# Kernel optimization log

Measured on AMD Instinct MI355X. Metric: run time of the kernel, lower is better.

## Reference

```python
import jax, jax.numpy as jnp
import numpy as np

N_LAYERS = 8
DILATIONS = [1, 2, 1, 2, 1, 2, 1, 2]
K_HOPS = 3
BN = 13248   # batch(64) * n_nodes(207), merged as in the torch module
L = 13       # 12 history steps + 1; shrinks by sum(dilations)=12 across layers
E = 211968   # BN * avg_degree(16)


def _conv1d(x, w, b, dil):
    # x: (BN, Cin, L), w: (Cout, Cin, 2) kernel-2 dilated conv, VALID (causal shrink)
    y = jax.lax.conv_general_dilated(x, w, (1,), 'VALID', rhs_dilation=(dil,),
                                     dimension_numbers=('NCH', 'OIH', 'NCH'))
    return y + b[None, :, None]


def setup_inputs() -> dict:
    key = jax.random.key(0)
    ks = jax.random.split(key, 20)
    s = 0.1  # keep activations in a sane range
    return {
        'x': jax.random.normal(ks[0], (BN, L, 2), jnp.float32),
        'edge_src': jax.random.randint(ks[1], (E,), 0, BN),
        'edge_dst': jax.random.randint(ks[2], (E,), 0, BN),
        'edge_w': jax.random.uniform(ks[3], (E,), jnp.float32),
        'init_w': s * jax.random.normal(ks[4], (2, 32), jnp.float32),
        'init_b': s * jax.random.normal(ks[5], (32,), jnp.float32),
        'filt_w': s * jax.random.normal(ks[6], (8, 32, 32, 2), jnp.float32),
        'filt_b': s * jax.random.normal(ks[7], (8, 32), jnp.float32),
        'gate_w': s * jax.random.normal(ks[8], (8, 32, 32, 2), jnp.float32),
        'gate_b': s * jax.random.normal(ks[9], (8, 32), jnp.float32),
        'gcn_w': s * jax.random.normal(ks[10], (8, 6, 32, 32), jnp.float32),
        'gcn_b': s * jax.random.normal(ks[11], (8, 32), jnp.float32),
        'skip_w': s * jax.random.normal(ks[12], (8, 256, 32), jnp.float32),
        'skip_b': s * jax.random.normal(ks[13], (8, 256), jnp.float32),
        'out0_w': s * jax.random.normal(ks[14], (256, 512), jnp.float32),
        'out0_b': s * jax.random.normal(ks[15], (512,), jnp.float32),
        'out1_w': s * jax.random.normal(ks[16], (512, 12), jnp.float32),
        'out1_b': s * jax.random.normal(ks[17], (12,), jnp.float32),
    }


def reference(x, edge_src, edge_dst, edge_w, init_w, init_b,
              filt_w, filt_b, gate_w, gate_b, gcn_w, gcn_b,
              skip_w, skip_b, out0_w, out0_b, out1_w, out1_b):
    # init linear: (BN, L, 2) -> (BN, L, 32) -> (BN, 32, L)
    h = (x @ init_w + init_b).transpose(0, 2, 1)
    # per-hop edge weights: elementwise powers of the transition weights
    # (faithful to repo's dense_to_sparse(transition ** k)); bck = transposed edges
    adjs = [(edge_src, edge_dst, edge_w ** k) for k in range(1, K_HOPS + 1)] + \
           [(edge_dst, edge_src, edge_w ** k) for k in range(1, K_HOPS + 1)]
    skip = None
    for l in range(N_LAYERS):
        d = DILATIONS[l]
        res = h
        # Gated TCN: tanh(filter) * sigmoid(gate), seq shrinks by d
        t = jnp.tanh(_conv1d(h, filt_w[l], filt_b[l], d)) * \
            jax.nn.sigmoid(_conv1d(h, gate_w[l], gate_b[l], d))
        # Diffusion conv: sum over 6 adjacency types of A_w (x W_a)
        xt = t.transpose(0, 2, 1)  # (BN, L', 32)
        g = jnp.zeros_like(xt)
        for a, (src, dst, w) in enumerate(adjs):
            msg = (xt @ gcn_w[l, a])[src] * w[:, None, None]  # (E, L', 32)
            g = g + jax.ops.segment_sum(msg, dst, num_segments=BN)
        h = g.transpose(0, 2, 1) + gcn_b[l][None, :, None]  # (BN, 32, L')
        # residual connection (align shrunk sequence)
        h = h + res[:, :, -h.shape[-1]:]
        # skip conv (1x1) on last timestep, accumulated
        sc = h[:, :, -1] @ skip_w[l].T + skip_b[l]  # (BN, 256)
        skip = sc if skip is None else skip + sc
    out = jax.nn.relu(skip)
    out = jax.nn.relu(out @ out0_w + out0_b)
    return out @ out1_w + out1_b  # (BN, 12)
```

## Files before the change

kernel.cpp:

```cpp
#include <hip/hip_runtime.h>

#define BN 13248
#define NE 211968

typedef __attribute__((ext_vector_type(8))) short bf16x8;
typedef __attribute__((ext_vector_type(4))) float f32x4;

__device__ __forceinline__ f32x4 mfma16(bf16x8 a, bf16x8 b, f32x4 c) {
  return __builtin_amdgcn_mfma_f32_16x16x32_bf16(a, b, c, 0, 0, 0);
}

__device__ __forceinline__ unsigned short to_bf16(float v) {
  unsigned bits = __float_as_uint(v);
  return (unsigned short)((bits + 0x7FFFu + ((bits >> 16) & 1u)) >> 16);
}

__device__ __forceinline__ float fast_tanh(float x) {
  float e2 = __expf(2.f * x);
  return 1.f - 2.f / (e2 + 1.f);
}
__device__ __forceinline__ float fast_sig(float x) {
  return 1.f / (1.f + __expf(-x));
}

__global__ void k_count(const int* __restrict__ src, const int* __restrict__ dst,
                        int* __restrict__ cur_f, int* __restrict__ cur_b) {
  int e = blockIdx.x * 256 + threadIdx.x;
  if (e < NE) {
    atomicAdd(&cur_f[dst[e]], 1);
    atomicAdd(&cur_b[src[e]], 1);
  }
}

__global__ void k_scan(int* __restrict__ cur_f, int* __restrict__ row_f,
                       int* __restrict__ cur_b, int* __restrict__ row_b) {
  __shared__ int sdata[1024];
  int tid = threadIdx.x;
  for (int which = 0; which < 2; ++which) {
    int* cnt = which ? cur_b : cur_f;
    int* row = which ? row_b : row_f;
    int base = tid * 13;
    int vals[13];
    int tot = 0;
    for (int k = 0; k < 13; ++k) {
      int idx = base + k;
      int v = (idx < BN) ? cnt[idx] : 0;
      vals[k] = v; tot += v;
    }
    sdata[tid] = tot;
    __syncthreads();
    for (int off = 1; off < 1024; off <<= 1) {
      int add = (tid >= off) ? sdata[tid - off] : 0;
      __syncthreads();
      sdata[tid] += add;
      __syncthreads();
    }
    int running = sdata[tid] - tot;
    for (int k = 0; k < 13; ++k) {
      int idx = base + k;
      if (idx < BN) { row[idx] = running; cnt[idx] = running; running += vals[k]; }
    }
    if (tid == 1023) row[BN] = sdata[1023];
    __syncthreads();
  }
}

__global__ void k_fill(const int* __restrict__ src, const int* __restrict__ dst,
                       const float* __restrict__ w,
                       int* __restrict__ cur_f, int2* __restrict__ ce_f,
                       int* __restrict__ cur_b, int2* __restrict__ ce_b) {
  int e = blockIdx.x * 256 + threadIdx.x;
  if (e < NE) {
    int s = src[e], t = dst[e];
    int wb = __float_as_int(w[e]);
    int p = atomicAdd(&cur_f[t], 1); ce_f[p] = make_int2(s, wb);
    int q = atomicAdd(&cur_b[s], 1); ce_b[q] = make_int2(t, wb);
  }
}

__global__ void k_init(const float* __restrict__ x, const float* __restrict__ iw,
                       const float* __restrict__ ib, float* __restrict__ h) {
  int idx = blockIdx.x * 256 + threadIdx.x;
  if (idx >= BN * 13 * 32) return;
  int c = idx & 31;
  int r = idx >> 5;
  int n = r % BN;
  int tau = r / BN;
  float x0 = x[(n * 13 + tau) * 2 + 0];
  float x1 = x[(n * 13 + tau) * 2 + 1];
  h[idx] = fmaf(x0, iw[c], fmaf(x1, iw[32 + c], ib[c]));
}

__global__ void k_pack(const float* __restrict__ skip_w, const float* __restrict__ skip_b,
                       const float* __restrict__ w0, const float* __restrict__ w1,
                       const float* __restrict__ gcn_w,
                       unsigned short* __restrict__ SWb, unsigned short* __restrict__ W0T,
                       unsigned short* __restrict__ W1T, float* __restrict__ bsum,
                       unsigned short* __restrict__ GgT) {
  int id = blockIdx.x * 256 + threadIdx.x;
  if (id < 65536) {
    int j = id >> 8, k = id & 255;
    SWb[id] = to_bf16(skip_w[((k >> 5) * 256 + j) * 32 + (k & 31)]);
  }
  if (id < 131072) {
    int jo = id >> 8, k = id & 255;
    W0T[id] = to_bf16(w0[k * 512 + jo]);
  }
  if (id < 8192) {
    int n = id >> 9, k = id & 511;
    W1T[id] = (n < 12) ? to_bf16(w1[k * 12 + n]) : (unsigned short)0;
  }
  if (id < 256) {
    float s = 0.f;
    for (int l = 0; l < 8; ++l) s += skip_b[l * 256 + id];
    bsum[id] = s;
  }
  if (id < 49152) {
    int l = id / 6144, rem = id % 6144;
    int co = rem / 192, k = rem % 192;
    int a = k >> 5, ci = k & 31;
    GgT[id] = to_bf16(gcn_w[((l * 6 + a) * 32 + ci) * 32 + co]);
  }
}

template<int LIN, int D, int TPAD>
__global__ __launch_bounds__(256) void k_tcn(const float* __restrict__ h_in, unsigned short* __restrict__ t_out,
    const float* __restrict__ fw, const float* __restrict__ fb,
    const float* __restrict__ gw, const float* __restrict__ gb) {
  constexpr int LOUT = LIN - D;
  __shared__ __align__(16) float wq[32 * 32 * 4];
  __shared__ float hl[8][LIN * 32];
  int tid = threadIdx.x;
  for (int f = tid; f < 4096; f += 256) {
    int e = f & 3, co = (f >> 2) & 31, ci = f >> 7;
    const float* srcw = (e < 2) ? fw : gw;
    wq[f] = srcw[(co * 32 + ci) * 2 + (e & 1)];
  }
  int n0 = blockIdx.x * 8;
  for (int i = tid; i < 8 * LIN * 32; i += 256) {
    int c = i & 31, r = i >> 5;
    int nl = r / LIN, tau = r % LIN;
    hl[nl][tau * 32 + c] = h_in[(tau * BN + n0 + nl) * 32 + c];
  }
  __syncthreads();
  int nl = tid >> 5, co = tid & 31;
  int n = n0 + nl;
  float accf[LOUT], accg[LOUT];
  float fbv = fb[co], gbv = gb[co];
#pragma unroll
  for (int j = 0; j < LOUT; ++j) { accf[j] = fbv; accg[j] = gbv; }
#pragma unroll
  for (int ci = 0; ci < 32; ++ci) {
    float4 wv = *(const float4*)&wq[(ci * 32 + co) * 4];
    float xr[LIN];
#pragma unroll
    for (int t = 0; t < LIN; ++t) xr[t] = hl[nl][t * 32 + ci];
#pragma unroll
    for (int j = 0; j < LOUT; ++j) {
      accf[j] = fmaf(xr[j], wv.x, accf[j]);
      accf[j] = fmaf(xr[j + D], wv.y, accf[j]);
      accg[j] = fmaf(xr[j], wv.z, accg[j]);
      accg[j] = fmaf(xr[j + D], wv.w, accg[j]);
    }
  }
#pragma unroll
  for (int j = 0; j < TPAD; ++j) {
    float v = (j < LOUT) ? fast_tanh(accf[j < LOUT ? j : 0]) * fast_sig(accg[j < LOUT ? j : 0]) : 0.f;
    t_out[(n * TPAD + j) * 32 + co] = (j < LOUT) ? to_bf16(v) : (unsigned short)0;
  }
}

__device__ __forceinline__ void bf4_fma3(uint2 u, float w1, float w2, float w3,
                                         float4* A0, float4* A1, float4* A2) {
  float v0 = __uint_as_float(u.x << 16);
  float v1 = __uint_as_float(u.x & 0xFFFF0000u);
  float v2 = __uint_as_float(u.y << 16);
  float v3 = __uint_as_float(u.y & 0xFFFF0000u);
  A0->x = fmaf(w1, v0, A0->x); A0->y = fmaf(w1, v1, A0->y);
  A0->z = fmaf(w1, v2, A0->z); A0->w = fmaf(w1, v3, A0->w);
  A1->x = fmaf(w2, v0, A1->x); A1->y = fmaf(w2, v1, A1->y);
  A1->z = fmaf(w2, v2, A1->z); A1->w = fmaf(w2, v3, A1->w);
  A2->x = fmaf(w3, v0, A2->x); A2->y = fmaf(w3, v1, A2->y);
  A2->z = fmaf(w3, v2, A2->z); A2->w = fmaf(w3, v3, A2->w);
}

template<int TPAD, int NT>
__device__ __forceinline__ void gather_dir(const unsigned short* __restrict__ t_in,
    int e0, int e1, const int2* __restrict__ ce, int rowoff0, float4 (*A)[NT]) {
  constexpr int EB = (NT >= 3) ? 2 : 4;
  int e = e0;
  for (; e + EB <= e1; e += EB) {
    int2 c[EB];
    uint2 u[EB][NT];
#pragma unroll
    for (int k = 0; k < EB; ++k) c[k] = ce[e + k];
#pragma unroll
    for (int k = 0; k < EB; ++k) {
      const unsigned short* p = t_in + c[k].x * (TPAD * 32) + rowoff0;
#pragma unroll
      for (int j = 0; j < NT; ++j) u[k][j] = *(const uint2*)(p + j * 32);
    }
#pragma unroll
    for (int k = 0; k < EB; ++k) {
      float w1 = __int_as_float(c[k].y);
      float w2 = w1 * w1, w3 = w2 * w1;
#pragma unroll
      for (int j = 0; j < NT; ++j)
        bf4_fma3(u[k][j], w1, w2, w3, &A[0][j], &A[1][j], &A[2][j]);
    }
  }
  for (; e < e1; ++e) {
    int2 c = ce[e];
    float w1 = __int_as_float(c.y);
    float w2 = w1 * w1, w3 = w2 * w1;
    const unsigned short* p = t_in + c.x * (TPAD * 32) + rowoff0;
#pragma unroll
    for (int j = 0; j < NT; ++j) {
      uint2 u = *(const uint2*)(p + j * 32);
      bf4_fma3(u, w1, w2, w3, &A[0][j], &A[1][j], &A[2][j]);
    }
  }
}

#define ZSTRIDE 200

template<int LOUT, int D, int TPAD>
__global__ __launch_bounds__(128, 4) void k_agg(const unsigned short* __restrict__ t_in,
    const float* __restrict__ h_in, float* __restrict__ h_out, float* __restrict__ lastcol,
    const int* __restrict__ row_f, const int2* __restrict__ ce_f,
    const int* __restrict__ row_b, const int2* __restrict__ ce_b,
    const unsigned short* __restrict__ WgT,
    const float* __restrict__ bias) {
  constexpr int NT = TPAD / 4;
  __shared__ __align__(16) unsigned short Zl[4 * TPAD * ZSTRIDE];
  int tid = threadIdx.x;
  int nl = tid >> 5, lane32 = tid & 31;
  int tl = lane32 >> 3;
  int c4 = (lane32 & 7) << 2;
  int n0 = blockIdx.x * 4;
  int n = n0 + nl;
  int rowoff0 = (tl * NT) * 32 + c4;
  int ef0 = row_f[n], ef1 = row_f[n + 1];
  int eb0 = row_b[n], eb1 = row_b[n + 1];
  float4 accf[3][NT], accb[3][NT];
#pragma unroll
  for (int a = 0; a < 3; ++a)
#pragma unroll
    for (int j = 0; j < NT; ++j) {
      accf[a][j] = make_float4(0.f, 0.f, 0.f, 0.f);
      accb[a][j] = make_float4(0.f, 0.f, 0.f, 0.f);
    }
  gather_dir<TPAD, NT>(t_in, ef0, ef1, ce_f, rowoff0, accf);
  gather_dir<TPAD, NT>(t_in, eb0, eb1, ce_b, rowoff0, accb);
#pragma unroll
  for (int j = 0; j < NT; ++j) {
    int m = nl * TPAD + tl * NT + j;
#pragma unroll
    for (int a = 0; a < 3; ++a) {
      ushort4 pf, pb;
      pf.x = to_bf16(accf[a][j].x); pf.y = to_bf16(accf[a][j].y);
      pf.z = to_bf16(accf[a][j].z); pf.w = to_bf16(accf[a][j].w);
      pb.x = to_bf16(accb[a][j].x); pb.y = to_bf16(accb[a][j].y);
      pb.z = to_bf16(accb[a][j].z); pb.w = to_bf16(accb[a][j].w);
      *(ushort4*)(&Zl[m * ZSTRIDE + a * 32 + c4]) = pf;
      *(ushort4*)(&Zl[m * ZSTRIDE + (a + 3) * 32 + c4]) = pb;
    }
  }
  __syncthreads();
  int wave = tid >> 6, lane = tid & 63;
  int m16 = lane & 15, q = lane >> 4;
#pragma unroll
  for (int i = 0; i < NT; ++i) {
    int u = wave * NT + i;
    int mt = u >> 1, nt = u & 1;
    f32x4 dacc = (f32x4){0.f, 0.f, 0.f, 0.f};
#pragma unroll
    for (int ks = 0; ks < 6; ++ks) {
      bf16x8 av = *(const bf16x8*)(&Zl[(mt * 16 + m16) * ZSTRIDE + ks * 32 + q * 8]);
      bf16x8 bv = *(const bf16x8*)(WgT + (nt * 16 + m16) * 192 + ks * 32 + q * 8);
      dacc = mfma16(av, bv, dacc);
    }
    int co = nt * 16 + m16;
    float bco = bias[co];
#pragma unroll
    for (int r = 0; r < 4; ++r) {
      int mm = mt * 16 + q * 4 + r;
      int node = n0 + mm / TPAD;
      int tau = mm % TPAD;
      if (tau < LOUT) {
        float rres = h_in[((tau + D) * BN + node) * 32 + co];
        float o = dacc[r] + bco + rres;
        h_out[(tau * BN + node) * 32 + co] = o;
        if (tau == LOUT - 1) lastcol[node * 32 + co] = o;
      }
    }
  }
}

__device__ __forceinline__ bf16x8 ldsA(const unsigned short* buf, int stride, int row, int ks, int q) {
  int unit = ks * 4 + q;
  int addr = row * stride + ((unit ^ (row & 7)) << 3);
  return *(const bf16x8*)(buf + addr);
}

__global__ __launch_bounds__(256) void k_final(const float* __restrict__ lastcol,
    const unsigned short* __restrict__ SWb, const unsigned short* __restrict__ W0T,
    const unsigned short* __restrict__ W1T, const float* __restrict__ bsum,
    const float* __restrict__ b0, const float* __restrict__ b1,
    float* __restrict__ out) {
  __shared__ __align__(16) unsigned short Z[32 * 256];
  __shared__ __align__(16) unsigned short H[32 * 512];
  int tid = threadIdx.x;
  int wave = tid >> 6, lane = tid & 63;
  int m16 = lane & 15, q = lane >> 4;
  int n0 = blockIdx.x * 32;
#pragma unroll
  for (int it = 0; it < 32; ++it) {
    int id = it * 256 + tid;
    int m = id >> 8, k = id & 255;
    float v = lastcol[((k >> 5) * BN + n0 + m) * 32 + (k & 31)];
    Z[m * 256 + (((k >> 3) ^ (m & 7)) << 3) + (k & 7)] = to_bf16(v);
  }
  __syncthreads();
  f32x4 acc1[2][4];
#pragma unroll
  for (int mt = 0; mt < 2; ++mt)
#pragma unroll
    for (int i = 0; i < 4; ++i) acc1[mt][i] = (f32x4){0.f, 0.f, 0.f, 0.f};
#pragma unroll
  for (int ks = 0; ks < 8; ++ks) {
    bf16x8 a0 = ldsA(Z, 256, m16, ks, q);
    bf16x8 a1 = ldsA(Z, 256, 16 + m16, ks, q);
#pragma unroll
    for (int i = 0; i < 4; ++i) {
      int j = (wave * 4 + i) * 16 + m16;
      bf16x8 b = *(const bf16x8*)(SWb + j * 256 + ks * 32 + q * 8);
      acc1[0][i] = mfma16(a0, b, acc1[0][i]);
      acc1[1][i] = mfma16(a1, b, acc1[1][i]);
    }
  }
  __syncthreads();
#pragma unroll
  for (int i = 0; i < 4; ++i) {
    int j = (wave * 4 + i) * 16 + m16;
    float bs = bsum[j];
#pragma unroll
    for (int mt = 0; mt < 2; ++mt)
#pragma unroll
      for (int r = 0; r < 4; ++r) {
        int row = mt * 16 + q * 4 + r;
        float v = fmaxf(acc1[mt][i][r] + bs, 0.f);
        Z[row * 256 + (((j >> 3) ^ (row & 7)) << 3) + (j & 7)] = to_bf16(v);
      }
  }
  __syncthreads();
  f32x4 acc2[2][8];
#pragma unroll
  for (int mt = 0; mt < 2; ++mt)
#pragma unroll
    for (int i = 0; i < 8; ++i) acc2[mt][i] = (f32x4){0.f, 0.f, 0.f, 0.f};
#pragma unroll
  for (int ks = 0; ks < 8; ++ks) {
    bf16x8 a0 = ldsA(Z, 256, m16, ks, q);
    bf16x8 a1 = ldsA(Z, 256, 16 + m16, ks, q);
#pragma unroll
    for (int i = 0; i < 8; ++i) {
      int jo = (wave * 8 + i) * 16 + m16;
      bf16x8 b = *(const bf16x8*)(W0T + jo * 256 + ks * 32 + q * 8);
      acc2[0][i] = mfma16(a0, b, acc2[0][i]);
      acc2[1][i] = mfma16(a1, b, acc2[1][i]);
    }
  }
#pragma unroll
  for (int i = 0; i < 8; ++i) {
    int jo = (wave * 8 + i) * 16 + m16;
    float b0v = b0[jo];
#pragma unroll
    for (int mt = 0; mt < 2; ++mt)
#pragma unroll
      for (int r = 0; r < 4; ++r) {
        int row = mt * 16 + q * 4 + r;
        float v = fmaxf(acc2[mt][i][r] + b0v, 0.f);
        H[row * 512 + (((jo >> 3) ^ (row & 7)) << 3) + (jo & 7)] = to_bf16(v);
      }
  }
  __syncthreads();
  if (wave < 2) {
    f32x4 acc3 = (f32x4){0.f, 0.f, 0.f, 0.f};
#pragma unroll
    for (int ks = 0; ks < 16; ++ks) {
      bf16x8 a = ldsA(H, 512, wave * 16 + m16, ks, q);
      bf16x8 b = *(const bf16x8*)(W1T + m16 * 512 + ks * 32 + q * 8);
      acc3 = mfma16(a, b, acc3);
    }
    if (m16 < 12) {
      float bv = b1[m16];
#pragma unroll
      for (int r = 0; r < 4; ++r)
        out[(n0 + wave * 16 + q * 4 + r) * 12 + m16] = acc3[r] + bv;
    }
  }
}

extern "C" void kernel_launch(void* const* d_in, const int* in_sizes, int n_in,
                              void* d_out, int out_size, void* d_ws, size_t ws_size,
                              hipStream_t stream) {
  const float* x      = (const float*)d_in[0];
  const int*   esrc   = (const int*)d_in[1];
  const int*   edst   = (const int*)d_in[2];
  const float* ew     = (const float*)d_in[3];
  const float* init_w = (const float*)d_in[4];
  const float* init_b = (const float*)d_in[5];
  const float* filt_w = (const float*)d_in[6];
  const float* filt_b = (const float*)d_in[7];
  const float* gate_w = (const float*)d_in[8];
  const float* gate_b = (const float*)d_in[9];
  const float* gcn_w  = (const float*)d_in[10];
  const float* gcn_b  = (const float*)d_in[11];
  const float* skip_w = (const float*)d_in[12];
  const float* skip_b = (const float*)d_in[13];
  const float* w0     = (const float*)d_in[14];
  const float* b0     = (const float*)d_in[15];
  const float* w1     = (const float*)d_in[16];
  const float* b1     = (const float*)d_in[17];
  float* out = (float*)d_out;

  float* base = (float*)d_ws;
  float* hA      = base;
  float* hB      = hA + 13 * BN * 32;
  float* tbuf    = hB + 13 * BN * 32;
  float* lastcol = tbuf + 12 * BN * 32;
  int* row_f = (int*)(lastcol + 8 * BN * 32);
  int* row_b = row_f + (BN + 1);
  int* cur_f = row_b + (BN + 1);
  int* cur_b = cur_f + BN;
  int2* ce_f = (int2*)(cur_b + BN);
  int2* ce_b = ce_f + NE;
  unsigned short* tbuf_u = (unsigned short*)tbuf;
  unsigned short* SWb = tbuf_u + 16 * BN * 32;
  unsigned short* W0T = SWb + 65536;
  unsigned short* W1T = W0T + 131072;
  float* bsumv = (float*)(W1T + 8192);
  unsigned short* GgT = (unsigned short*)(bsumv + 256);

  hipMemsetAsync(cur_f, 0, 2 * BN * sizeof(int), stream);
  const int egrid = (NE + 255) / 256;
  k_count<<<egrid, 256, 0, stream>>>(esrc, edst, cur_f, cur_b);
  k_scan<<<1, 1024, 0, stream>>>(cur_f, row_f, cur_b, row_b);
  k_fill<<<egrid, 256, 0, stream>>>(esrc, edst, ew, cur_f, ce_f, cur_b, ce_b);
  k_init<<<(BN * 13 * 32 + 255) / 256, 256, 0, stream>>>(x, init_w, init_b, hA);
  k_pack<<<512, 256, 0, stream>>>(skip_w, skip_b, w0, w1, gcn_w, SWb, W0T, W1T, bsumv, GgT);

#define LAYER(l, LIN, DD, TP, hin, hout) \
  k_tcn<LIN, DD, TP><<<BN / 8, 256, 0, stream>>>(hin, tbuf_u, filt_w + l * 2048, filt_b + l * 32, \
                                                 gate_w + l * 2048, gate_b + l * 32); \
  k_agg<LIN - DD, DD, TP><<<BN / 4, 128, 0, stream>>>(tbuf_u, hin, hout, \
      lastcol + l * BN * 32, row_f, ce_f, row_b, ce_b, GgT + l * 6144, gcn_b + l * 32);

  LAYER(0, 13, 1, 12, hA, hB)
  LAYER(1, 12, 2, 12, hB, hA)
  LAYER(2, 10, 1, 12, hA, hB)
  LAYER(3,  9, 2,  8, hB, hA)
  LAYER(4,  7, 1,  8, hA, hB)
  LAYER(5,  6, 2,  4, hB, hA)
  LAYER(6,  4, 1,  4, hA, hB)
  LAYER(7,  3, 2,  4, hB, hA)
#undef LAYER

  k_final<<<BN / 32, 256, 0, stream>>>(lastcol, SWb, W0T, W1T, bsumv, b0, b1, out);
}
```

Before: 759.7 us.

## Fuse next-layer TCN into aggregation kernel and switch gather to packed fp16

Each aggregation kernel now computes the gated TCN of the following layer from the freshly produced h values kept in shared memory. This removes seven separate TCN launches and the global re-read of h. Intermediate t activations and GCN weights move from bf16 to fp16, and the edge gather accumulates with packed half2 FMAs instead of fp32, halving the ALU work per edge. The cost is fp16 accumulation over many edges, which risks precision loss or overflow, more shared memory, and fewer resident blocks because launch bounds drop to 2.

Measured after the change: 740.3 us. -2.6%, faster.

```diff
diff --git a/kernel.cpp b/kernel.cpp
--- a/kernel.cpp
+++ b/kernel.cpp
@@ -1,18 +1,33 @@
 #include <hip/hip_runtime.h>
+#include <hip/hip_fp16.h>
 
 #define BN 13248
 #define NE 211968
+#define ZSTRIDE 200
 
 typedef __attribute__((ext_vector_type(8))) short bf16x8;
+typedef __attribute__((ext_vector_type(8))) _Float16 f16x8;
 typedef __attribute__((ext_vector_type(4))) float f32x4;
 
-__device__ __forceinline__ f32x4 mfma16(bf16x8 a, bf16x8 b, f32x4 c) {
+__device__ __forceinline__ f32x4 mfma16b(bf16x8 a, bf16x8 b, f32x4 c) {
   return __builtin_amdgcn_mfma_f32_16x16x32_bf16(a, b, c, 0, 0, 0);
+}
+__device__ __forceinline__ f32x4 mfma16h(f16x8 a, f16x8 b, f32x4 c) {
+  return __builtin_amdgcn_mfma_f32_16x16x32_f16(a, b, c, 0, 0, 0);
 }
 
 __device__ __forceinline__ unsigned short to_bf16(float v) {
   unsigned bits = __float_as_uint(v);
   return (unsigned short)((bits + 0x7FFFu + ((bits >> 16) & 1u)) >> 16);
+}
+__device__ __forceinline__ unsigned short to_f16(float v) {
+  union { __half h; unsigned short s; } u; u.h = __float2half(v); return u.s;
+}
+__device__ __forceinline__ unsigned h2u(__half2 h) {
+  union { __half2 h; unsigned u; } v; v.h = h; return v.u;
+}
+__device__ __forceinline__ __half2 u2h(unsigned u) {
+  union { unsigned u; __half2 h; } v; v.u = u; return v.h;
 }
 
 __device__ __forceinline__ float fast_tanh(float x) {
@@ -94,9 +109,10 @@
 __global__ void k_pack(const float* __restrict__ skip_w, const float* __restrict__ skip_b,
                        const float* __restrict__ w0, const float* __restrict__ w1,
                        const float* __restrict__ gcn_w,
+                       const float* __restrict__ filt_w, const float* __restrict__ gate_w,
                        unsigned short* __restrict__ SWb, unsigned short* __restrict__ W0T,
                        unsigned short* __restrict__ W1T, float* __restrict__ bsum,
-                       unsigned short* __restrict__ GgT) {
+                       unsigned short* __restrict__ Gg16, uint2* __restrict__ WQ2) {
   int id = blockIdx.x * 256 + threadIdx.x;
   if (id < 65536) {
     int j = id >> 8, k = id & 255;
@@ -119,7 +135,17 @@
     int l = id / 6144, rem = id % 6144;
     int co = rem / 192, k = rem % 192;
     int a = k >> 5, ci = k & 31;
-    GgT[id] = to_bf16(gcn_w[((l * 6 + a) * 32 + ci) * 32 + co]);
+    Gg16[id] = to_f16(gcn_w[((l * 6 + a) * 32 + ci) * 32 + co]);
+  }
+  if (id < 7168) {
+    int l = id / 1024 + 1, rem = id % 1024;
+    int ci = rem >> 5, co = rem & 31;
+    const float* fw = filt_w + l * 2048;
+    const float* gw = gate_w + l * 2048;
+    __half2 a, b;
+    a.x = __float2half(fw[(co * 32 + ci) * 2 + 0]); a.y = __float2half(gw[(co * 32 + ci) * 2 + 0]);
+    b.x = __float2half(fw[(co * 32 + ci) * 2 + 1]); b.y = __float2half(gw[(co * 32 + ci) * 2 + 1]);
+    WQ2[id] = make_uint2(h2u(a), h2u(b));
   }
 }
 
@@ -165,29 +191,16 @@
   }
 #pragma unroll
   for (int j = 0; j < TPAD; ++j) {
-    float v = (j < LOUT) ? fast_tanh(accf[j < LOUT ? j : 0]) * fast_sig(accg[j < LOUT ? j : 0]) : 0.f;
-    t_out[(n * TPAD + j) * 32 + co] = (j < LOUT) ? to_bf16(v) : (unsigned short)0;
-  }
-}
-
-__device__ __forceinline__ void bf4_fma3(uint2 u, float w1, float w2, float w3,
-                                         float4* A0, float4* A1, float4* A2) {
-  float v0 = __uint_as_float(u.x << 16);
-  float v1 = __uint_as_float(u.x & 0xFFFF0000u);
-  float v2 = __uint_as_float(u.y << 16);
-  float v3 = __uint_as_float(u.y & 0xFFFF0000u);
-  A0->x = fmaf(w1, v0, A0->x); A0->y = fmaf(w1, v1, A0->y);
-  A0->z = fmaf(w1, v2, A0->z); A0->w = fmaf(w1, v3, A0->w);
-  A1->x = fmaf(w2, v0, A1->x); A1->y = fmaf(w2, v1, A1->y);
-  A1->z = fmaf(w2, v2, A1->z); A1->w = fmaf(w2, v3, A1->w);
-  A2->x = fmaf(w3, v0, A2->x); A2->y = fmaf(w3, v1, A2->y);
-  A2->z = fmaf(w3, v2, A2->z); A2->w = fmaf(w3, v3, A2->w);
+    unsigned short v = 0;
+    if (j < LOUT) v = to_f16(fast_tanh(accf[j < LOUT ? j : 0]) * fast_sig(accg[j < LOUT ? j : 0]));
+    t_out[(n * TPAD + j) * 32 + co] = v;
+  }
 }
 
 template<int TPAD, int NT>
 __device__ __forceinline__ void gather_dir(const unsigned short* __restrict__ t_in,
-    int e0, int e1, const int2* __restrict__ ce, int rowoff0, float4 (*A)[NT]) {
-  constexpr int EB = (NT >= 3) ? 2 : 4;
+    int e0, int e1, const int2* __restrict__ ce, int rowoff0, __half2* A) {
+  constexpr int EB = 4;
   int e = e0;
   for (; e + EB <= e1; e += EB) {
     int2 c[EB];
@@ -202,38 +215,60 @@
     }
 #pragma unroll
     for (int k = 0; k < EB; ++k) {
-      float w1 = __int_as_float(c[k].y);
-      float w2 = w1 * w1, w3 = w2 * w1;
-#pragma unroll
-      for (int j = 0; j < NT; ++j)
-        bf4_fma3(u[k][j], w1, w2, w3, &A[0][j], &A[1][j], &A[2][j]);
+      float w1 = __int_as_float(c[k].y), w2 = w1 * w1, w3 = w2 * w1;
+      __half2 wh0 = __float2half2_rn(w1), wh1 = __float2half2_rn(w2), wh2 = __float2half2_rn(w3);
+#pragma unroll
+      for (int j = 0; j < NT; ++j) {
+        __half2 v0 = u2h(u[k][j].x), v1 = u2h(u[k][j].y);
+        A[(0 * NT + j) * 2 + 0] = __hfma2(wh0, v0, A[(0 * NT + j) * 2 + 0]);
+        A[(0 * NT + j) * 2 + 1] = __hfma2(wh0, v1, A[(0 * NT + j) * 2 + 1]);
+        A[(1 * NT + j) * 2 + 0] = __hfma2(wh1, v0, A[(1 * NT + j) * 2 + 0]);
+        A[(1 * NT + j) * 2 + 1] = __hfma2(wh1, v1, A[(1 * NT + j) * 2 + 1]);
+        A[(2 * NT + j) * 2 + 0] = __hfma2(wh2, v0, A[(2 * NT + j) * 2 + 0]);
+        A[(2 * NT + j) * 2 + 1] = __hfma2(wh2, v1, A[(2 * NT + j) * 2 + 1]);
+      }
     }
   }
   for (; e < e1; ++e) {
     int2 c = ce[e];
-    float w1 = __int_as_float(c.y);
-    float w2 = w1 * w1, w3 = w2 * w1;
+    float w1 = __int_as_float(c.y), w2 = w1 * w1, w3 = w2 * w1;
+    __half2 wh0 = __float2half2_rn(w1), wh1 = __float2half2_rn(w2), wh2 = __float2half2_rn(w3);
     const unsigned short* p = t_in + c.x * (TPAD * 32) + rowoff0;
 #pragma unroll
     for (int j = 0; j < NT; ++j) {
       uint2 u = *(const uint2*)(p + j * 32);
-      bf4_fma3(u, w1, w2, w3, &A[0][j], &A[1][j], &A[2][j]);
-    }
-  }
-}
-
-#define ZSTRIDE 200
-
-template<int LOUT, int D, int TPAD>
-__global__ __launch_bounds__(128, 4) void k_agg(const unsigned short* __restrict__ t_in,
-    const float* __restrict__ h_in, float* __restrict__ h_out, float* __restrict__ lastcol,
+      __half2 v0 = u2h(u.x), v1 = u2h(u.y);
+      A[(0 * NT + j) * 2 + 0] = __hfma2(wh0, v0, A[(0 * NT + j) * 2 + 0]);
+      A[(0 * NT + j) * 2 + 1] = __hfma2(wh0, v1, A[(0 * NT + j) * 2 + 1]);
+      A[(1 * NT + j) * 2 + 0] = __hfma2(wh1, v0, A[(1 * NT + j) * 2 + 0]);
+      A[(1 * NT + j) * 2 + 1] = __hfma2(wh1, v1, A[(1 * NT + j) * 2 + 1]);
+      A[(2 * NT + j) * 2 + 0] = __hfma2(wh2, v0, A[(2 * NT + j) * 2 + 0]);
+      A[(2 * NT + j) * 2 + 1] = __hfma2(wh2, v1, A[(2 * NT + j) * 2 + 1]);
+    }
+  }
+}
+
+template<int LOUT, int D, int TPAD, int D2, int TPAD2, bool LAST>
+__global__ __launch_bounds__(128, 2) void k_fused(
+    const unsigned short* __restrict__ t_in,
+    const float* __restrict__ h_in, float* __restrict__ h_out,
+    float* __restrict__ lastcol, unsigned short* __restrict__ t_next,
     const int* __restrict__ row_f, const int2* __restrict__ ce_f,
     const int* __restrict__ row_b, const int2* __restrict__ ce_b,
-    const unsigned short* __restrict__ WgT,
-    const float* __restrict__ bias) {
+    const unsigned short* __restrict__ Wg,
+    const float* __restrict__ bias,
+    const uint2* __restrict__ WQn,
+    const float* __restrict__ fbn, const float* __restrict__ gbn) {
   constexpr int NT = TPAD / 4;
+  constexpr int LIN2 = LOUT;
+  constexpr int LOUT2 = LAST ? 1 : (LOUT - D2);
   __shared__ __align__(16) unsigned short Zl[4 * TPAD * ZSTRIDE];
+  __shared__ __align__(16) uint2 wq2s[1024];
+  __shared__ float hbuf[4 * LIN2 * 33];
   int tid = threadIdx.x;
+  if (!LAST) {
+    for (int i = tid; i < 1024; i += 128) wq2s[i] = WQn[i];
+  }
   int nl = tid >> 5, lane32 = tid & 31;
   int tl = lane32 >> 3;
   int c4 = (lane32 & 7) << 2;
@@ -242,28 +277,19 @@
   int rowoff0 = (tl * NT) * 32 + c4;
   int ef0 = row_f[n], ef1 = row_f[n + 1];
   int eb0 = row_b[n], eb1 = row_b[n + 1];
-  float4 accf[3][NT], accb[3][NT];
-#pragma unroll
-  for (int a = 0; a < 3; ++a)
-#pragma unroll
-    for (int j = 0; j < NT; ++j) {
-      accf[a][j] = make_float4(0.f, 0.f, 0.f, 0.f);
-      accb[a][j] = make_float4(0.f, 0.f, 0.f, 0.f);
-    }
-  gather_dir<TPAD, NT>(t_in, ef0, ef1, ce_f, rowoff0, accf);
-  gather_dir<TPAD, NT>(t_in, eb0, eb1, ce_b, rowoff0, accb);
+  __half2 acc[6 * NT * 2];
+  __half2 zero = __float2half2_rn(0.f);
+#pragma unroll
+  for (int i = 0; i < 6 * NT * 2; ++i) acc[i] = zero;
+  gather_dir<TPAD, NT>(t_in, ef0, ef1, ce_f, rowoff0, acc);
+  gather_dir<TPAD, NT>(t_in, eb0, eb1, ce_b, rowoff0, acc + 3 * NT * 2);
 #pragma unroll
   for (int j = 0; j < NT; ++j) {
     int m = nl * TPAD + tl * NT + j;
 #pragma unroll
-    for (int a = 0; a < 3; ++a) {
-      ushort4 pf, pb;
-      pf.x = to_bf16(accf[a][j].x); pf.y = to_bf16(accf[a][j].y);
-      pf.z = to_bf16(accf[a][j].z); pf.w = to_bf16(accf[a][j].w);
-      pb.x = to_bf16(accb[a][j].x); pb.y = to_bf16(accb[a][j].y);
-      pb.z = to_bf16(accb[a][j].z); pb.w = to_bf16(accb[a][j].w);
-      *(ushort4*)(&Zl[m * ZSTRIDE + a * 32 + c4]) = pf;
-      *(ushort4*)(&Zl[m * ZSTRIDE + (a + 3) * 32 + c4]) = pb;
+    for (int a = 0; a < 6; ++a) {
+      uint2 v = make_uint2(h2u(acc[(a * NT + j) * 2 + 0]), h2u(acc[(a * NT + j) * 2 + 1]));
+      *(uint2*)(&Zl[m * ZSTRIDE + a * 32 + c4]) = v;
     }
   }
   __syncthreads();
@@ -276,9 +302,9 @@
     f32x4 dacc = (f32x4){0.f, 0.f, 0.f, 0.f};
 #pragma unroll
     for (int ks = 0; ks < 6; ++ks) {
-      bf16x8 av = *(const bf16x8*)(&Zl[(mt * 16 + m16) * ZSTRIDE + ks * 32 + q * 8]);
-      bf16x8 bv = *(const bf16x8*)(WgT + (nt * 16 + m16) * 192 + ks * 32 + q * 8);
-      dacc = mfma16(av, bv, dacc);
+      f16x8 av = *(const f16x8*)(&Zl[(mt * 16 + m16) * ZSTRIDE + ks * 32 + q * 8]);
+      f16x8 bv = *(const f16x8*)((const _Float16*)Wg + (nt * 16 + m16) * 192 + ks * 32 + q * 8);
+      dacc = mfma16h(av, bv, dacc);
     }
     int co = nt * 16 + m16;
     float bco = bias[co];
@@ -291,8 +317,41 @@
         float rres = h_in[((tau + D) * BN + node) * 32 + co];
         float o = dacc[r] + bco + rres;
         h_out[(tau * BN + node) * 32 + co] = o;
+        hbuf[(mm / TPAD) * (LIN2 * 33) + tau * 33 + co] = o;
         if (tau == LOUT - 1) lastcol[node * 32 + co] = o;
       }
+    }
+  }
+  if (!LAST) {
+    __syncthreads();
+    int co = lane32;
+    float accf[LOUT2], accg[LOUT2];
+    float fbv = fbn[co], gbv = gbn[co];
+#pragma unroll
+    for (int j = 0; j < LOUT2; ++j) { accf[j] = fbv; accg[j] = gbv; }
+    const float* hb = &hbuf[nl * (LIN2 * 33)];
+#pragma unroll
+    for (int ci = 0; ci < 32; ++ci) {
+      uint2 wp = wq2s[ci * 32 + co];
+      __half2 wa = u2h(wp.x), wb = u2h(wp.y);
+      float wf0 = __low2float(wa), wg0 = __high2float(wa);
+      float wf1 = __low2float(wb), wg1 = __high2float(wb);
+      float xr[LIN2];
+#pragma unroll
+      for (int t = 0; t < LIN2; ++t) xr[t] = hb[t * 33 + ci];
+#pragma unroll
+      for (int j = 0; j < LOUT2; ++j) {
+        accf[j] = fmaf(xr[j], wf0, accf[j]);
+        accf[j] = fmaf(xr[j + D2], wf1, accf[j]);
+        accg[j] = fmaf(xr[j], wg0, accg[j]);
+        accg[j] = fmaf(xr[j + D2], wg1, accg[j]);
+      }
+    }
+#pragma unroll
+    for (int j = 0; j < TPAD2; ++j) {
+      unsigned short v = 0;
+      if (j < LOUT2) v = to_f16(fast_tanh(accf[j < LOUT2 ? j : 0]) * fast_sig(accg[j < LOUT2 ? j : 0]));
+      t_next[(n * TPAD2 + j) * 32 + co] = v;
     }
   }
 }
@@ -335,8 +394,8 @@
     for (int i = 0; i < 4; ++i) {
       int j = (wave * 4 + i) * 16 + m16;
       bf16x8 b = *(const bf16x8*)(SWb + j * 256 + ks * 32 + q * 8);
-      acc1[0][i] = mfma16(a0, b, acc1[0][i]);
-      acc1[1][i] = mfma16(a1, b, acc1[1][i]);
+      acc1[0][i] = mfma16b(a0, b, acc1[0][i]);
+      acc1[1][i] = mfma16b(a1, b, acc1[1][i]);
     }
   }
   __syncthreads();
@@ -367,8 +426,8 @@
     for (int i = 0; i < 8; ++i) {
       int jo = (wave * 8 + i) * 16 + m16;
       bf16x8 b = *(const bf16x8*)(W0T + jo * 256 + ks * 32 + q * 8);
-      acc2[0][i] = mfma16(a0, b, acc2[0][i]);
-      acc2[1][i] = mfma16(a1, b, acc2[1][i]);
+      acc2[0][i] = mfma16b(a0, b, acc2[0][i]);
+      acc2[1][i] = mfma16b(a1, b, acc2[1][i]);
     }
   }
 #pragma unroll
@@ -391,7 +450,7 @@
     for (int ks = 0; ks < 16; ++ks) {
       bf16x8 a = ldsA(H, 512, wave * 16 + m16, ks, q);
       bf16x8 b = *(const bf16x8*)(W1T + m16 * 512 + ks * 32 + q * 8);
-      acc3 = mfma16(a, b, acc3);
+      acc3 = mfma16b(a, b, acc3);
     }
     if (m16 < 12) {
       float bv = b1[m16];
@@ -428,20 +487,21 @@
   float* base = (float*)d_ws;
   float* hA      = base;
   float* hB      = hA + 13 * BN * 32;
-  float* tbuf    = hB + 13 * BN * 32;
-  float* lastcol = tbuf + 12 * BN * 32;
+  unsigned short* tA = (unsigned short*)(hB + 13 * BN * 32);
+  unsigned short* tB = tA + 12 * BN * 32;
+  float* lastcol = (float*)(tB + 12 * BN * 32);
   int* row_f = (int*)(lastcol + 8 * BN * 32);
-  int* row_b = row_f + (BN + 1);
-  int* cur_f = row_b + (BN + 1);
+  int* row_b = row_f + (BN + 2);
+  int* cur_f = row_b + (BN + 2);
   int* cur_b = cur_f + BN;
   int2* ce_f = (int2*)(cur_b + BN);
   int2* ce_b = ce_f + NE;
-  unsigned short* tbuf_u = (unsigned short*)tbuf;
-  unsigned short* SWb = tbuf_u + 16 * BN * 32;
-  unsigned short* W0T = SWb + 65536;
-  unsigned short* W1T = W0T + 131072;
-  float* bsumv = (float*)(W1T + 8192);
-  unsigned short* GgT = (unsigned short*)(bsumv + 256);
+  unsigned short* SWb  = (unsigned short*)(ce_b + NE);
+  unsigned short* W0T  = SWb + 65536;
+  unsigned short* W1T  = W0T + 131072;
+  unsigned short* Gg16 = W1T + 8192;
+  uint2* WQ2   = (uint2*)(Gg16 + 49152);
+  float* bsumv = (float*)(WQ2 + 7168);
 
   hipMemsetAsync(cur_f, 0, 2 * BN * sizeof(int), stream);
   const int egrid = (NE + 255) / 256;
@@ -449,23 +509,27 @@
   k_scan<<<1, 1024, 0, stream>>>(cur_f, row_f, cur_b, row_b);
   k_fill<<<egrid, 256, 0, stream>>>(esrc, edst, ew, cur_f, ce_f, cur_b, ce_b);
   k_init<<<(BN * 13 * 32 + 255) / 256, 256, 0, stream>>>(x, init_w, init_b, hA);
-  k_pack<<<512, 256, 0, stream>>>(skip_w, skip_b, w0, w1, gcn_w, SWb, W0T, W1T, bsumv, GgT);
-
-#define LAYER(l, LIN, DD, TP, hin, hout) \
-  k_tcn<LIN, DD, TP><<<BN / 8, 256, 0, stream>>>(hin, tbuf_u, filt_w + l * 2048, filt_b + l * 32, \
-                                                 gate_w + l * 2048, gate_b + l * 32); \
-  k_agg<LIN - DD, DD, TP><<<BN / 4, 128, 0, stream>>>(tbuf_u, hin, hout, \
-      lastcol + l * BN * 32, row_f, ce_f, row_b, ce_b, GgT + l * 6144, gcn_b + l * 32);
-
-  LAYER(0, 13, 1, 12, hA, hB)
-  LAYER(1, 12, 2, 12, hB, hA)
-  LAYER(2, 10, 1, 12, hA, hB)
-  LAYER(3,  9, 2,  8, hB, hA)
-  LAYER(4,  7, 1,  8, hA, hB)
-  LAYER(5,  6, 2,  4, hB, hA)
-  LAYER(6,  4, 1,  4, hA, hB)
-  LAYER(7,  3, 2,  4, hB, hA)
-#undef LAYER
+  k_pack<<<512, 256, 0, stream>>>(skip_w, skip_b, w0, w1, gcn_w, filt_w, gate_w,
+                                  SWb, W0T, W1T, bsumv, Gg16, WQ2);
+
+  k_tcn<13, 1, 12><<<BN / 8, 256, 0, stream>>>(hA, tA, filt_w, filt_b, gate_w, gate_b);
+
+#define FUSED(l, LOUTv, Dv, TPv, D2v, TP2v, LASTv, tin, tout, hin, hout) \
+  k_fused<LOUTv, Dv, TPv, D2v, TP2v, LASTv><<<BN / 4, 128, 0, stream>>>( \
+      tin, hin, hout, lastcol + l * BN * 32, tout, row_f, ce_f, row_b, ce_b, \
+      Gg16 + l * 6144, gcn_b + l * 32, WQ2 + l * 1024, filt_b + (l + 1) * 32, gate_b + (l + 1) * 32);
+
+  FUSED(0, 12, 1, 12, 2, 12, false, tA, tB, hA, hB)
+  FUSED(1, 10, 2, 12, 1, 12, false, tB, tA, hB, hA)
+  FUSED(2,  9, 1, 12, 2,  8, false, tA, tB, hA, hB)
+  FUSED(3,  7, 2,  8, 1,  8, false, tB, tA, hB, hA)
+  FUSED(4,  6, 1,  8, 2,  4, false, tA, tB, hA, hB)
+  FUSED(5,  4, 2,  4, 1,  4, false, tB, tA, hB, hA)
+  FUSED(6,  3, 1,  4, 2,  4, false, tA, tB, hA, hB)
+#undef FUSED
+  k_fused<1, 2, 4, 2, 4, true><<<BN / 4, 128, 0, stream>>>(
+      tB, hB, hA, lastcol + 7 * BN * 32, tA, row_f, ce_f, row_b, ce_b,
+      Gg16 + 7 * 6144, gcn_b + 7 * 32, WQ2, filt_b, gate_b);
 
   k_final<<<BN / 32, 256, 0, stream>>>(lastcol, SWb, W0T, W1T, bsumv, b0, b1, out);
 }
```
